# Performance work log

Measured on AMD Instinct MI355X. Metric: run time of the kernel, lower is better.

## Reference

```python
import jax, jax.numpy as jnp
import numpy as np

CHUNK_LEN = 32
N_HEAD = 32
HEAD_SIZE = 64
EPS = 1e-5 * 64.0  # GroupNorm eps = 1e-5 * head_size_divisor**2
PREC_MIN = 0.005   # rwkv_inner precision_min_val clamp for fp32


def rwkv_inner(r, k, v, w, u, kv_state, chunk_len):
    # r,k,v,w: [B,H,L,K]; u: [H,K]; kv_state: [B,H,K,V]
    B, H, L, K = k.shape
    T = chunk_len
    N = L // T
    w = jnp.clip(w, PREC_MIN, None)
    wc_log = jnp.log(w).reshape(B, H, N, T, K)
    wc_cum = jnp.cumsum(wc_log, axis=-2)                      # [B,H,N,T,K]
    shifted = jnp.concatenate([jnp.zeros_like(wc_cum[..., :1, :]), wc_cum[..., :-1, :]], axis=-2)
    ws_log = jnp.sum(wc_log, axis=-2, keepdims=True)          # [B,H,N,1,K]
    w_inter = jnp.exp(ws_log - wc_cum)                        # decay to end of chunk
    w_intra = jnp.exp(wc_cum - wc_log)                        # decay from start of chunk
    rc = r.reshape(B, H, N, T, K)
    kc = k.reshape(B, H, N, T, K)
    vc = v.reshape(B, H, N, T, K)
    # intra-chunk attention, log-space offset at T//2 for numerical stability
    off = shifted[..., T // 2:T // 2 + 1, :]
    r_decay = jnp.exp(shifted - off)
    k_inv_decay = jnp.exp(off - wc_cum)
    a = jnp.einsum('bhntk,bhnsk->bhnts', rc * r_decay, kc * k_inv_decay)
    a = jnp.tril(a, -1)
    diag = jnp.einsum('bhntk,bhntk->bhnt', rc, u[None, :, None, None, :] * kc)
    out = jnp.einsum('bhnts,bhnsv->bhntv', a, vc) + diag[..., None] * vc
    # per-chunk (k*w_inter)^T @ v contributions, then sequential state carry
    wkv = jnp.einsum('bhntk,bhntv->bhnkv', kc * w_inter, vc)  # [B,H,N,K,V]
    ws = jnp.exp(ws_log)[:, :, :, 0, :]                       # [B,H,N,K]

    def step(state, xs):
        ws_i, wkv_i = xs
        new_state = state * ws_i[..., None] + wkv_i
        return new_state, state

    final_state, states = jax.lax.scan(step, kv_state, (jnp.moveaxis(ws, 2, 0), jnp.moveaxis(wkv, 2, 0)))
    states = jnp.moveaxis(states, 0, 2)                       # [B,H,N,K,V]
    out = out + jnp.einsum('bhntk,bhnkv->bhntv', rc * w_intra, states)
    return out.reshape(B, H, L, K), final_state


def _forward(x, shift_state, wkv_state,
             time_maa_x, time_maa_w, time_maa_k, time_maa_v, time_maa_r, time_maa_g,
             time_maa_w1, time_maa_w2, time_decay, time_decay_w1, time_decay_w2,
             time_faaaa, Wr, Wk, Wv, Wg, Wo, gn_w, gn_b):
    B, T, C = x.shape
    H, K = N_HEAD, HEAD_SIZE
    xprev = jnp.concatenate([shift_state[:, None, :], x[:, :-1]], axis=1)
    dx = xprev - x
    # token-shift LoRA mixing
    xxx = jnp.tanh((x + dx * time_maa_x) @ time_maa_w1).reshape(B, T, 5, -1)
    m = jnp.einsum('btfe,fec->fbtc', xxx, time_maa_w2)  # [5,B,T,C]
    mw, mk, mv, mr, mg = m[0], m[1], m[2], m[3], m[4]
    xk = x + dx * (time_maa_k + mk)
    xv = x + dx * (time_maa_v + mv)
    xr = x + dx * (time_maa_r + mr)
    xg = x + dx * (time_maa_g + mg)
    xw = x + dx * (time_maa_w + mw)
    r = (xr @ Wr.T).reshape(B, T, H, K).transpose(0, 2, 1, 3)
    k = (xk @ Wk.T).reshape(B, T, H, K).transpose(0, 2, 1, 3)
    v = (xv @ Wv.T).reshape(B, T, H, K).transpose(0, 2, 1, 3)
    g = jax.nn.silu(xg @ Wg.T)
    w = time_decay.reshape(1, H, 1, K) + (jnp.tanh(xw @ time_decay_w1) @ time_decay_w2).reshape(B, T, H, K).transpose(0, 2, 1, 3)
    w = jnp.exp(-jnp.exp(w))
    out, wkv_out = rwkv_inner(r, k, v, w, time_faaaa, wkv_state, CHUNK_LEN)
    out = out.transpose(0, 2, 1, 3).reshape(B, T, C)
    # GroupNorm with H groups of K channels
    og = out.reshape(B, T, H, K)
    mu = og.mean(-1, keepdims=True)
    var = og.var(-1, keepdims=True)
    og = (og - mu) * jax.lax.rsqrt(var + EPS)
    out = og.reshape(B, T, C) * gn_w + gn_b
    out = (out * g) @ Wo.T
    return out, x[:, -1], wkv_out


def setup_inputs() -> dict:
    B, T, C = 4, 2048, 2048
    H, K = N_HEAD, HEAD_SIZE
    E5, TD = 32, 64
    key = jax.random.key(0)
    ks = jax.random.split(key, 24)
    f32 = jnp.float32
    inp = {
        'x': jax.random.normal(ks[0], (B, T, C), f32),
        'shift_state': jax.random.normal(ks[1], (B, C), f32),
        'wkv_state': jax.random.normal(ks[2], (B, H, K, K), f32) * 0.1,
        'time_maa_x': jax.random.uniform(ks[3], (1, 1, C), f32),
        'time_maa_w': jax.random.uniform(ks[4], (1, 1, C), f32),
        'time_maa_k': jax.random.uniform(ks[5], (1, 1, C), f32),
        'time_maa_v': jax.random.uniform(ks[6], (1, 1, C), f32),
        'time_maa_r': jax.random.uniform(ks[7], (1, 1, C), f32),
        'time_maa_g': jax.random.uniform(ks[8], (1, 1, C), f32),
        'time_maa_w1': jax.random.uniform(ks[9], (C, E5 * 5), f32, -1e-4, 1e-4),
        'time_maa_w2': jax.random.normal(ks[10], (5, E5, C), f32) * 0.01,
        'time_decay': jnp.linspace(-6.0, -1.0, C, dtype=f32).reshape(1, 1, C),
        'time_decay_w1': jax.random.uniform(ks[11], (C, TD), f32, -1e-4, 1e-4),
        'time_decay_w2': jax.random.normal(ks[12], (TD, C), f32) * 0.01,
        'time_faaaa': jax.random.normal(ks[13], (H, K), f32) * 0.1,
        'Wr': jax.random.normal(ks[14], (C, C), f32) * 0.02,
        'Wk': jax.random.normal(ks[15], (C, C), f32) * 0.02,
        'Wv': jax.random.normal(ks[16], (C, C), f32) * 0.02,
        'Wg': jax.random.normal(ks[17], (C, C), f32) * 0.02,
        'Wo': jax.random.normal(ks[18], (C, C), f32) * 0.02,
        'gn_w': jnp.ones((C,), f32),
        'gn_b': jnp.zeros((C,), f32),
    }
    return inp


def reference(x, shift_state, wkv_state,
              time_maa_x, time_maa_w, time_maa_k, time_maa_v, time_maa_r, time_maa_g,
              time_maa_w1, time_maa_w2, time_decay, time_decay_w1, time_decay_w2,
              time_faaaa, Wr, Wk, Wv, Wg, Wo, gn_w, gn_b):
    return _forward(x, shift_state, wkv_state,
                    time_maa_x, time_maa_w, time_maa_k, time_maa_v, time_maa_r, time_maa_g,
                    time_maa_w1, time_maa_w2, time_decay, time_decay_w1, time_decay_w2,
                    time_faaaa, Wr, Wk, Wv, Wg, Wo, gn_w, gn_b)
```

## Files before the change

### kernel.cpp

```cpp
#include <hip/hip_runtime.h>
#include <stdint.h>
#include <math.h>


typedef __attribute__((ext_vector_type(8))) short bf16x8;
typedef __attribute__((ext_vector_type(4))) float f32x4;

#define AS1(p) ((const __attribute__((address_space(1))) void*)(p))
#define AS3(p) ((__attribute__((address_space(3))) void*)(p))

__device__ __forceinline__ unsigned short f2bf(float f) {
  unsigned int u = __builtin_bit_cast(unsigned int, f);
  u += 0x7fffu + ((u >> 16) & 1u);
  return (unsigned short)(u >> 16);
}
__device__ __forceinline__ float bf2f(unsigned short s) {
  unsigned int u = ((unsigned int)s) << 16;
  return __builtin_bit_cast(float, u);
}

template <int EPI, bool BOUNDS>
__global__ __launch_bounds__(256) void gemm_nt(
    const unsigned short* __restrict__ A, const unsigned short* __restrict__ B,
    void* __restrict__ Cp, int M, int N, int K, const float* __restrict__ evec,
    int slot)
{
  __shared__ __align__(16) unsigned short As[128 * 32];
  __shared__ __align__(16) unsigned short Bs[128 * 32];
  const int tid = threadIdx.x;
  const int l = tid & 63, w = tid >> 6;
  const int wm = w & 1, wn = w >> 1;
  const int lm = l & 15, quad = l >> 4;
  const long mBase = (long)blockIdx.y * 128;
  const long nBase = (long)blockIdx.x * 128;

  f32x4 acc[4][4];
  f32x4 zero = {0.f, 0.f, 0.f, 0.f};
#pragma unroll
  for (int i = 0; i < 4; i++)
#pragma unroll
    for (int j = 0; j < 4; j++) acc[i][j] = zero;

  for (int k0 = 0; k0 < K; k0 += 32) {
    if (!BOUNDS) {
      const int r0 = w * 32;
      const int lr = l >> 2, lc = l & 3;
      const unsigned short* gA = A + (mBase + r0 + lr) * (long)K + k0 + lc * 8;
      __builtin_amdgcn_global_load_lds(AS1(gA), AS3(&As[r0 * 32]), 16, 0, 0);
      const unsigned short* gA2 = gA + 16 * (long)K;
      __builtin_amdgcn_global_load_lds(AS1(gA2), AS3(&As[(r0 + 16) * 32]), 16, 0, 0);
      const unsigned short* gB = B + (nBase + r0 + lr) * (long)K + k0 + lc * 8;
      __builtin_amdgcn_global_load_lds(AS1(gB), AS3(&Bs[r0 * 32]), 16, 0, 0);
      const unsigned short* gB2 = gB + 16 * (long)K;
      __builtin_amdgcn_global_load_lds(AS1(gB2), AS3(&Bs[(r0 + 16) * 32]), 16, 0, 0);
    } else {
      const int row = tid >> 2, ch = tid & 3;
#pragma unroll
      for (int rr = 0; rr < 128; rr += 64) {
        int r = rr + row;
        *(int4*)&As[r * 32 + ch * 8] =
            *(const int4*)&A[(mBase + r) * (long)K + k0 + ch * 8];
        int4 bv = make_int4(0, 0, 0, 0);
        long nG = nBase + r;
        if (nG < N) bv = *(const int4*)&B[nG * (long)K + k0 + ch * 8];
        *(int4*)&Bs[r * 32 + ch * 8] = bv;
      }
    }
    __syncthreads();
    bf16x8 af[4], bq[4];
#pragma unroll
    for (int i = 0; i < 4; i++)
      af[i] = *(const bf16x8*)&As[(wm * 64 + i * 16 + lm) * 32 + quad * 8];
#pragma unroll
    for (int i = 0; i < 4; i++)
      bq[i] = *(const bf16x8*)&Bs[(wn * 64 + i * 16 + lm) * 32 + quad * 8];
#pragma unroll
    for (int mi = 0; mi < 4; mi++)
#pragma unroll
      for (int ni = 0; ni < 4; ni++)
        acc[mi][ni] = __builtin_amdgcn_mfma_f32_16x16x32_bf16(af[mi], bq[ni], acc[mi][ni], 0, 0, 0);
    __syncthreads();
  }

#pragma unroll
  for (int mi = 0; mi < 4; mi++) {
#pragma unroll
    for (int ni = 0; ni < 4; ni++) {
      long col = nBase + wn * 64 + ni * 16 + lm;
      if (BOUNDS && col >= N) continue;
      long rw0 = mBase + wm * 64 + mi * 16 + quad * 4;
#pragma unroll
      for (int r = 0; r < 4; r++) {
        float y = acc[mi][ni][r];
        long row = rw0 + r;
        long off = row * (long)N + col;
        if constexpr (EPI == 0) {
          ((float*)Cp)[off] = y;
        } else if constexpr (EPI == 2) {
          ((unsigned short*)Cp)[off] = f2bf(tanhf(y));
        } else if constexpr (EPI == 3) {
          ((unsigned short*)Cp)[off] = f2bf(y / (1.f + __expf(-y)));
        } else if constexpr (EPI == 4) {
          float wv = evec[col] + y;
          ((_Float16*)Cp)[off] = (_Float16)fmaxf(-__expf(wv), -5.2983174f);
        } else if constexpr (EPI == 5) {
          int b = (int)(row >> 11), t = (int)(row & 2047);
          int n = t >> 5, tt = t & 31;
          int h = (int)(col >> 6), kk = (int)(col & 63);
          long c = ((long)(b * 32 + h)) * 64 + n;
          ((unsigned short*)Cp)[c * 6144 + slot + tt * 64 + kk] = f2bf(y);
        }
      }
    }
  }
}

__global__ __launch_bounds__(256) void k_convert(const float* __restrict__ s,
                                                 unsigned short* __restrict__ d, int n4)
{
  int i = blockIdx.x * 256 + threadIdx.x;
  if (i >= n4) return;
  float4 v = ((const float4*)s)[i];
  short4 o;
  o.x = (short)f2bf(v.x); o.y = (short)f2bf(v.y);
  o.z = (short)f2bf(v.z); o.w = (short)f2bf(v.w);
  ((short4*)d)[i] = o;
}

__global__ __launch_bounds__(256) void k_transpose(const float* __restrict__ s,
                                                   unsigned short* __restrict__ d, int R, int C)
{
  int i = blockIdx.x * 256 + threadIdx.x;
  if (i >= R * C) return;
  int r = i / C, c = i - r * C;
  d[(long)c * R + r] = f2bf(s[i]);
}

__global__ __launch_bounds__(256) void k_prep(const float* __restrict__ x,
                                              const float* __restrict__ shift,
                                              const float* __restrict__ maax,
                                              unsigned short* __restrict__ xmix,
                                              float* __restrict__ xlast)
{
  int i = blockIdx.x * 256 + threadIdx.x;
  int c4 = (i & 511) * 4;
  long bt = i >> 9;
  int t = (int)(bt & 2047);
  long b = bt >> 11;
  float4 xv = *(const float4*)&x[bt * 2048 + c4];
  float4 xp;
  if (t == 0) xp = *(const float4*)&shift[b * 2048 + c4];
  else        xp = *(const float4*)&x[(bt - 1) * 2048 + c4];
  float4 mx = *(const float4*)&maax[c4];
  short4 o;
  o.x = (short)f2bf(xv.x + (xp.x - xv.x) * mx.x);
  o.y = (short)f2bf(xv.y + (xp.y - xv.y) * mx.y);
  o.z = (short)f2bf(xv.z + (xp.z - xv.z) * mx.z);
  o.w = (short)f2bf(xv.w + (xp.w - xv.w) * mx.w);
  *(short4*)&xmix[bt * 2048 + c4] = o;
  if (t == 2047) *(float4*)&xlast[b * 2048 + c4] = xv;
}

__global__ __launch_bounds__(256) void k_mix1(
    const unsigned short* __restrict__ xxx, const unsigned short* __restrict__ w2t,
    const float* __restrict__ x, const float* __restrict__ shift,
    const float* __restrict__ maa, unsigned short* __restrict__ xout, int f)
{
  __shared__ __align__(16) unsigned short As[128 * 32];
  __shared__ __align__(16) unsigned short Bs[128 * 32];
  const int tid = threadIdx.x;
  const int l = tid & 63, w = tid >> 6;
  const int wm = w & 1, wn = w >> 1;
  const int lm = l & 15, quad = l >> 4;
  const long mBase = (long)blockIdx.y * 128;
  const long nBase = (long)blockIdx.x * 128;
  const int row = tid >> 2, ch = tid & 3;
#pragma unroll
  for (int rr = 0; rr < 128; rr += 64) {
    int r = rr + row;
    *(int4*)&As[r * 32 + ch * 8] =
        *(const int4*)&xxx[(mBase + r) * 160 + f * 32 + ch * 8];
    *(int4*)&Bs[r * 32 + ch * 8] =
        *(const int4*)&w2t[((long)f * 2048 + nBase + r) * 32 + ch * 8];
  }
  __syncthreads();
  f32x4 zero = {0.f, 0.f, 0.f, 0.f};
  f32x4 acc[4][4];
#pragma unroll
  for (int i = 0; i < 4; i++)
#pragma unroll
    for (int j = 0; j < 4; j++) acc[i][j] = zero;
  bf16x8 af[4], bq[4];
#pragma unroll
  for (int i = 0; i < 4; i++)
    af[i] = *(const bf16x8*)&As[(wm * 64 + i * 16 + lm) * 32 + quad * 8];
#pragma unroll
  for (int i = 0; i < 4; i++)
    bq[i] = *(const bf16x8*)&Bs[(wn * 64 + i * 16 + lm) * 32 + quad * 8];
#pragma unroll
  for (int mi = 0; mi < 4; mi++)
#pragma unroll
    for (int ni = 0; ni < 4; ni++)
      acc[mi][ni] = __builtin_amdgcn_mfma_f32_16x16x32_bf16(af[mi], bq[ni], acc[mi][ni], 0, 0, 0);

#pragma unroll
  for (int mi = 0; mi < 4; mi++) {
#pragma unroll
    for (int ni = 0; ni < 4; ni++) {
      long col = nBase + wn * 64 + ni * 16 + lm;
#pragma unroll
      for (int r = 0; r < 4; r++) {
        long rg = mBase + wm * 64 + mi * 16 + quad * 4 + r;
        int t = (int)(rg & 2047);
        long b = rg >> 11;
        float xval = x[rg * 2048 + col];
        float xp = t ? x[(rg - 1) * 2048 + col] : shift[b * 2048 + col];
        float res = xval + (xp - xval) * (maa[col] + acc[mi][ni][r]);
        xout[rg * 2048 + col] = f2bf(res);
      }
    }
  }
}

__global__ __launch_bounds__(256) void k_chunk(
    unsigned short* __restrict__ recs, const _Float16* __restrict__ wl,
    const float* __restrict__ u, float* __restrict__ outw,
    float* __restrict__ wsb)
{
  const int chunk = blockIdx.x;
  const int n = chunk & 63, bh = chunk >> 6;
  const int h = bh & 31, b = bh >> 5;
  const int tid = threadIdx.x;
  const int lane = tid & 63, wvid = tid >> 6;
  const long rec = (long)chunk * 6144;
  const long tbase = ((long)(b * 2048 + n * 32)) * 2048 + h * 64;

  __shared__ float vc[32][65];
  __shared__ float wcum[32][65];
  __shared__ float rdec[32][65];
  __shared__ float kdec[32][65];
  __shared__ float amat[32][33];
  __shared__ float wsk[64];

  float rcr[8], kcr[8];
#pragma unroll
  for (int j = 0; j < 8; j++) {
    int t = wvid + 4 * j;
    long g = rec + t * 64 + lane;
    rcr[j] = bf2f(recs[g]);
    kcr[j] = bf2f(recs[g + 2048]);
    vc[t][lane] = bf2f(recs[g + 4096]);
    wcum[t][lane] = (float)wl[tbase + (long)t * 2048 + lane];
  }
  float uval = u[h * 64 + lane];
  __syncthreads();

  if (tid < 64) {
    float run = 0.f;
    for (int t = 0; t < 32; t++) { run += wcum[t][tid]; wcum[t][tid] = run; }
    wsk[tid] = run;
  }
  __syncthreads();

  const float offv = wcum[15][lane];
  const float wsv = wsk[lane];
  float rdr[8], kdr[8], klr[8], rwir[8], dpart[8];
#pragma unroll
  for (int j = 0; j < 8; j++) {
    int t = wvid + 4 * j;
    float cw = wcum[t][lane];
    float sh = t ? wcum[t - 1][lane] : 0.f;
    rwir[j] = rcr[j] * __expf(sh);
    rdr[j] = rcr[j] * __expf(sh - offv);
    kdr[j] = kcr[j] * __expf(offv - cw);
    klr[j] = kcr[j] * __expf(wsv - cw);
    dpart[j] = rcr[j] * uval * kcr[j];
  }
  __syncthreads();

#pragma unroll
  for (int j = 0; j < 8; j++) {
    int t = wvid + 4 * j;
    rdec[t][lane] = rdr[j];
    kdec[t][lane] = kdr[j];
    wcum[t][lane] = klr[j];
    recs[rec + 4096 + t * 64 + lane] = f2bf(rwir[j]);
  }
  if (tid < 64) wsb[(long)chunk * 64 + tid] = __expf(wsk[tid]);
  __syncthreads();

  {
    const int t0 = (tid >> 4) * 2, s0 = (tid & 15) * 2;
    float a00 = 0, a01 = 0, a10 = 0, a11 = 0;
    for (int kk = 0; kk < 64; kk++) {
      float r0 = rdec[t0][kk], r1 = rdec[t0 + 1][kk];
      float c0 = kdec[s0][kk], c1 = kdec[s0 + 1][kk];
      a00 += r0 * c0; a01 += r0 * c1; a10 += r1 * c0; a11 += r1 * c1;
    }
    amat[t0][s0]         = (s0     < t0)     ? a00 : 0.f;
    amat[t0][s0 + 1]     = (s0 + 1 < t0)     ? a01 : 0.f;
    amat[t0 + 1][s0]     = (s0     < t0 + 1) ? a10 : 0.f;
    amat[t0 + 1][s0 + 1] = (s0 + 1 < t0 + 1) ? a11 : 0.f;
  }
  __syncthreads();
#pragma unroll
  for (int j = 0; j < 8; j++) {
    float d = dpart[j];
#pragma unroll
    for (int m = 32; m; m >>= 1) d += __shfl_xor(d, m, 64);
    if (lane == 0) amat[wvid + 4 * j][wvid + 4 * j] = d;
  }
  __syncthreads();

  {
    const int t0 = (tid >> 4) * 2, v0 = (tid & 15) * 4;
    float o00 = 0, o01 = 0, o02 = 0, o03 = 0, o10 = 0, o11 = 0, o12 = 0, o13 = 0;
    for (int s = 0; s < 32; s++) {
      float a0 = amat[t0][s], a1 = amat[t0 + 1][s];
      float b0 = vc[s][v0], b1 = vc[s][v0 + 1], b2 = vc[s][v0 + 2], b3 = vc[s][v0 + 3];
      o00 += a0 * b0; o01 += a0 * b1; o02 += a0 * b2; o03 += a0 * b3;
      o10 += a1 * b0; o11 += a1 * b1; o12 += a1 * b2; o13 += a1 * b3;
    }
    float* p0 = &outw[tbase + (long)t0 * 2048 + v0];
    float* p1 = &outw[tbase + (long)(t0 + 1) * 2048 + v0];
    p0[0] = o00; p0[1] = o01; p0[2] = o02; p0[3] = o03;
    p1[0] = o10; p1[1] = o11; p1[2] = o12; p1[3] = o13;
  }

  {
    const int kk0 = (tid >> 4) * 4, v0 = (tid & 15) * 4;
    float a[4][4];
#pragma unroll
    for (int i = 0; i < 4; i++)
#pragma unroll
      for (int j = 0; j < 4; j++) a[i][j] = 0.f;
    for (int t = 0; t < 32; t++) {
      float w0 = wcum[t][kk0], w1 = wcum[t][kk0 + 1], w2 = wcum[t][kk0 + 2], w3 = wcum[t][kk0 + 3];
      float b0 = vc[t][v0], b1 = vc[t][v0 + 1], b2 = vc[t][v0 + 2], b3 = vc[t][v0 + 3];
      a[0][0] += w0 * b0; a[0][1] += w0 * b1; a[0][2] += w0 * b2; a[0][3] += w0 * b3;
      a[1][0] += w1 * b0; a[1][1] += w1 * b1; a[1][2] += w1 * b2; a[1][3] += w1 * b3;
      a[2][0] += w2 * b0; a[2][1] += w2 * b1; a[2][2] += w2 * b2; a[2][3] += w2 * b3;
      a[3][0] += w3 * b0; a[3][1] += w3 * b1; a[3][2] += w3 * b2; a[3][3] += w3 * b3;
    }
#pragma unroll
    for (int i = 0; i < 4; i++)
#pragma unroll
      for (int j = 0; j < 4; j++)
        recs[rec + (kk0 + i) * 64 + v0 + j] = f2bf(a[i][j]);
  }
}

__global__ __launch_bounds__(256) void k_scan(unsigned short* __restrict__ recs,
                                              const float* __restrict__ wsb,
                                              const float* __restrict__ kv0,
                                              float* __restrict__ finalst)
{
  const int bh = blockIdx.x >> 2;
  const int kq = blockIdx.x & 3;
  const int tid = threadIdx.x;
  float st[4];
  const long base = (long)bh * 4096 + kq * 1024;
#pragma unroll
  for (int j = 0; j < 4; j++) st[j] = kv0[base + j * 256 + tid];
  for (int n = 0; n < 64; n++) {
    const long cb = ((long)bh * 64 + n) * 6144 + kq * 1024;
    const long wb = ((long)bh * 64 + n) * 64 + kq * 16;
#pragma unroll
    for (int j = 0; j < 4; j++) {
      int i = j * 256 + tid;
      unsigned short* p = &recs[cb + i];
      float wv = bf2f(*p);
      *p = f2bf(st[j]);
      st[j] = st[j] * wsb[wb + (i >> 6)] + wv;
    }
  }
#pragma unroll
  for (int j = 0; j < 4; j++) finalst[base + j * 256 + tid] = st[j];
}

__global__ __launch_bounds__(256) void k_inter(const unsigned short* __restrict__ recs,
                                               float* __restrict__ outw)
{
  const int chunk = blockIdx.x;
  const int n = chunk & 63, bh = chunk >> 6;
  const int h = bh & 31, b = bh >> 5;
  const int tid = threadIdx.x;
  __shared__ float st[64][65];
  __shared__ float rw[32][65];
  const long rec = (long)chunk * 6144;
  for (int i = tid; i < 4096; i += 256) st[i >> 6][i & 63] = bf2f(recs[rec + i]);
  for (int i = tid; i < 2048; i += 256) rw[i >> 6][i & 63] = bf2f(recs[rec + 4096 + i]);
  __syncthreads();
  const long tbase = ((long)(b * 2048 + n * 32)) * 2048 + h * 64;
  const int t0 = (tid >> 4) * 2, v0 = (tid & 15) * 4;
  float o00 = 0, o01 = 0, o02 = 0, o03 = 0, o10 = 0, o11 = 0, o12 = 0, o13 = 0;
  for (int kk = 0; kk < 64; kk++) {
    float r0 = rw[t0][kk], r1 = rw[t0 + 1][kk];
    float s0 = st[kk][v0], s1 = st[kk][v0 + 1], s2 = st[kk][v0 + 2], s3 = st[kk][v0 + 3];
    o00 += r0 * s0; o01 += r0 * s1; o02 += r0 * s2; o03 += r0 * s3;
    o10 += r1 * s0; o11 += r1 * s1; o12 += r1 * s2; o13 += r1 * s3;
  }
  float* p0 = &outw[tbase + (long)t0 * 2048 + v0];
  float* p1 = &outw[tbase + (long)(t0 + 1) * 2048 + v0];
  p0[0] += o00; p0[1] += o01; p0[2] += o02; p0[3] += o03;
  p1[0] += o10; p1[1] += o11; p1[2] += o12; p1[3] += o13;
}

__global__ __launch_bounds__(256) void k_gnorm(const float* __restrict__ outw,
                                               const unsigned short* __restrict__ gb,
                                               const float* __restrict__ gnw,
                                               const float* __restrict__ gnb,
                                               unsigned short* __restrict__ aout)
{
  const int gid = blockIdx.x * 4 + (threadIdx.x >> 6);
  const int lane = threadIdx.x & 63;
  const long bt = gid >> 5;
  const int h = gid & 31;
  const int c = h * 64 + lane;
  const long off = bt * 2048 + c;
  float y = outw[off];
  float s = y, sq = y * y;
#pragma unroll
  for (int m = 32; m; m >>= 1) {
    s += __shfl_xor(s, m, 64);
    sq += __shfl_xor(sq, m, 64);
  }
  float mu = s * (1.f / 64.f);
  float var = sq * (1.f / 64.f) - mu * mu;
  float nrm = (y - mu) * rsqrtf(var + 6.4e-4f);
  float o = (nrm * gnw[c] + gnb[c]) * bf2f(gb[off]);
  aout[off] = f2bf(o);
}

extern "C" void kernel_launch(void* const* d_in, const int* in_sizes, int n_in,
                              void* d_out, int out_size, void* d_ws, size_t ws_size,
                              hipStream_t stream)
{
  const float* x     = (const float*)d_in[0];
  const float* shift = (const float*)d_in[1];
  const float* kv0   = (const float*)d_in[2];
  const float* maax  = (const float*)d_in[3];
  const float* maaw  = (const float*)d_in[4];
  const float* maak  = (const float*)d_in[5];
  const float* maav  = (const float*)d_in[6];
  const float* maar  = (const float*)d_in[7];
  const float* maag  = (const float*)d_in[8];
  const float* w1    = (const float*)d_in[9];
  const float* w2    = (const float*)d_in[10];
  const float* tdec  = (const float*)d_in[11];
  const float* tdw1  = (const float*)d_in[12];
  const float* tdw2  = (const float*)d_in[13];
  const float* u     = (const float*)d_in[14];
  const float* Wr    = (const float*)d_in[15];
  const float* Wk    = (const float*)d_in[16];
  const float* Wv    = (const float*)d_in[17];
  const float* Wg    = (const float*)d_in[18];
  const float* Wo    = (const float*)d_in[19];
  const float* gnw   = (const float*)d_in[20];
  const float* gnb   = (const float*)d_in[21];

  char* ws = (char*)d_ws;
  const size_t MB = 1048576;
  unsigned short* WbfR  = (unsigned short*)(ws + 0 * MB);
  unsigned short* WbfK  = (unsigned short*)(ws + 8 * MB);
  unsigned short* WbfV  = (unsigned short*)(ws + 16 * MB);
  unsigned short* WbfG  = (unsigned short*)(ws + 24 * MB);
  unsigned short* WbfO  = (unsigned short*)(ws + 32 * MB);
  unsigned short* w2tb  = (unsigned short*)(ws + 40 * MB);
  unsigned short* w1t   = (unsigned short*)(ws + 40 * MB + 655360);
  unsigned short* tdw1t = (unsigned short*)(ws + 40 * MB + 1310720);
  unsigned short* tdw2t = (unsigned short*)(ws + 40 * MB + 1572864);
  unsigned short* xxxb  = (unsigned short*)(ws + 40 * MB + 1835008);
  unsigned short* t1b   = (unsigned short*)(ws + 40 * MB + 4456448);
  float*          wsb   = (float*)(ws + 40 * MB + 5505024);
  unsigned short* xmixb = (unsigned short*)(ws + 48 * MB);
  _Float16*       wlb   = (_Float16*)(ws + 48 * MB);
  unsigned short* x1b   = (unsigned short*)(ws + 80 * MB);
  unsigned short* aob   = (unsigned short*)(ws + 80 * MB);
  unsigned short* recs  = (unsigned short*)(ws + 112 * MB);
  unsigned short* gbuf  = recs;

  float* outp    = (float*)d_out;
  float* xlast   = outp + 16777216;
  float* finalst = outp + 16777216 + 8192;

  k_convert<<<4096, 256, 0, stream>>>(Wr, WbfR, 1048576);
  k_convert<<<4096, 256, 0, stream>>>(Wk, WbfK, 1048576);
  k_convert<<<4096, 256, 0, stream>>>(Wv, WbfV, 1048576);
  k_convert<<<4096, 256, 0, stream>>>(Wg, WbfG, 1048576);
  k_convert<<<4096, 256, 0, stream>>>(Wo, WbfO, 1048576);
  k_transpose<<<1280, 256, 0, stream>>>(w1, w1t, 2048, 160);
  k_transpose<<<512, 256, 0, stream>>>(tdw1, tdw1t, 2048, 64);
  k_transpose<<<512, 256, 0, stream>>>(tdw2, tdw2t, 64, 2048);
  for (int f = 0; f < 5; f++)
    k_transpose<<<256, 256, 0, stream>>>(w2 + (long)f * 65536, w2tb + (long)f * 65536, 32, 2048);

  k_prep<<<16384, 256, 0, stream>>>(x, shift, maax, xmixb, xlast);
  gemm_nt<2, true><<<dim3(2, 64), 256, 0, stream>>>(xmixb, w1t, xxxb, 8192, 160, 2048, nullptr, 0);

  k_mix1<<<dim3(16, 64), 256, 0, stream>>>(xxxb, w2tb, x, shift, maaw, x1b, 0);
  gemm_nt<2, true><<<dim3(1, 64), 256, 0, stream>>>(x1b, tdw1t, t1b, 8192, 64, 2048, nullptr, 0);
  gemm_nt<4, false><<<dim3(16, 64), 256, 0, stream>>>(t1b, tdw2t, wlb, 8192, 2048, 64, tdec, 0);
  k_mix1<<<dim3(16, 64), 256, 0, stream>>>(xxxb, w2tb, x, shift, maak, x1b, 1);
  gemm_nt<5, false><<<dim3(16, 64), 256, 0, stream>>>(x1b, WbfK, recs, 8192, 2048, 2048, nullptr, 2048);
  k_mix1<<<dim3(16, 64), 256, 0, stream>>>(xxxb, w2tb, x, shift, maav, x1b, 2);
  gemm_nt<5, false><<<dim3(16, 64), 256, 0, stream>>>(x1b, WbfV, recs, 8192, 2048, 2048, nullptr, 4096);
  k_mix1<<<dim3(16, 64), 256, 0, stream>>>(xxxb, w2tb, x, shift, maar, x1b, 3);
  gemm_nt<5, false><<<dim3(16, 64), 256, 0, stream>>>(x1b, WbfR, recs, 8192, 2048, 2048, nullptr, 0);
  k_mix1<<<dim3(16, 64), 256, 0, stream>>>(xxxb, w2tb, x, shift, maag, x1b, 4);

  k_chunk<<<8192, 256, 0, stream>>>(recs, wlb, u, outp, wsb);
  k_scan<<<512, 256, 0, stream>>>(recs, wsb, kv0, finalst);
  k_inter<<<8192, 256, 0, stream>>>(recs, outp);

  gemm_nt<3, false><<<dim3(16, 64), 256, 0, stream>>>(x1b, WbfG, gbuf, 8192, 2048, 2048, nullptr, 0);
  k_gnorm<<<65536, 256, 0, stream>>>(outp, gbuf, gnw, gnb, aob);
  gemm_nt<0, false><<<dim3(16, 64), 256, 0, stream>>>(aob, WbfO, outp, 8192, 2048, 2048, nullptr, 0);
}
```

Measured before the change: 1.361 ms.

## Add 256x256-tile double-buffered GEMM kernel for the five large projections

Adds a new 512-thread GEMM kernel with 256x256 output tiles, a K-step of 64, and double-buffered LDS filled through direct global-to-LDS loads using a swizzled layout. It interleaves MFMA work with prefetch of the next stage and raises wave priority around the MFMA blocks. The R/K/V/G/O projection GEMMs now use it in place of the 128-tile kernel. The aim is more data reuse per tile and better overlap of loads with compute. The cost is high register and LDS use, which allows only one block per CU, and a grid of 256 blocks that may underfill the device.

```diff
diff --git a/kernel.cpp b/kernel.cpp
--- a/kernel.cpp
+++ b/kernel.cpp
@@ -108,6 +108,131 @@
           int n = t >> 5, tt = t & 31;
           int h = (int)(col >> 6), kk = (int)(col & 63);
           long c = ((long)(b * 32 + h)) * 64 + n;
+          ((unsigned short*)Cp)[c * 6144 + slot + tt * 64 + kk] = f2bf(y);
+        }
+      }
+    }
+  }
+}
+
+template <int EPI>
+__global__ __launch_bounds__(512, 1) void gemm256_nt(
+    const unsigned short* __restrict__ A, const unsigned short* __restrict__ B,
+    void* __restrict__ Cp, int M, int N, int K, int slot)
+{
+  __shared__ __align__(16) unsigned short As2[2][16384];
+  __shared__ __align__(16) unsigned short Bs2[2][16384];
+  const int tid = threadIdx.x;
+  const int l = tid & 63;
+  const int w = tid >> 6;
+  const int wm = w >> 2, wn = w & 3;
+  const int lm = l & 15, quad = l >> 4;
+  const long mBase = (long)blockIdx.y * 256;
+  const long nBase = (long)blockIdx.x * 256;
+  const int NT = K >> 6;
+
+  const int r0 = tid >> 3;
+  const int csw = (tid & 7) ^ (r0 & 7);
+  const int ldsOff = (tid & ~63) * 8;
+  const unsigned short* ga0 = A + (mBase + r0) * (long)K + csw * 8;
+  const unsigned short* gb0 = B + (nBase + r0) * (long)K + csw * 8;
+
+  f32x4 acc[8][4];
+  f32x4 zero = {0.f, 0.f, 0.f, 0.f};
+#pragma unroll
+  for (int i = 0; i < 8; i++)
+#pragma unroll
+    for (int j = 0; j < 4; j++) acc[i][j] = zero;
+
+#define STAGE256(kt_)                                                          \
+  {                                                                            \
+    const int _b = (kt_) & 1;                                                  \
+    const unsigned short* _ga = ga0 + (long)(kt_) * 64;                        \
+    const unsigned short* _gb = gb0 + (long)(kt_) * 64;                        \
+    __builtin_amdgcn_global_load_lds(AS1(_ga), AS3(&As2[_b][ldsOff]), 16, 0, 0);              \
+    __builtin_amdgcn_global_load_lds(AS1(_gb), AS3(&Bs2[_b][ldsOff]), 16, 0, 0);              \
+    __builtin_amdgcn_global_load_lds(AS1(_ga + (long)64 * K), AS3(&As2[_b][4096 + ldsOff]), 16, 0, 0);  \
+    __builtin_amdgcn_global_load_lds(AS1(_gb + (long)64 * K), AS3(&Bs2[_b][4096 + ldsOff]), 16, 0, 0);  \
+    __builtin_amdgcn_global_load_lds(AS1(_ga + (long)128 * K), AS3(&As2[_b][8192 + ldsOff]), 16, 0, 0); \
+    __builtin_amdgcn_global_load_lds(AS1(_gb + (long)128 * K), AS3(&Bs2[_b][8192 + ldsOff]), 16, 0, 0); \
+    __builtin_amdgcn_global_load_lds(AS1(_ga + (long)192 * K), AS3(&As2[_b][12288 + ldsOff]), 16, 0, 0);\
+    __builtin_amdgcn_global_load_lds(AS1(_gb + (long)192 * K), AS3(&Bs2[_b][12288 + ldsOff]), 16, 0, 0);\
+  }
+
+  STAGE256(0);
+  STAGE256(1);
+  asm volatile("s_waitcnt vmcnt(8)" ::: "memory");
+  __builtin_amdgcn_s_barrier();
+
+  const int q0 = (quad ^ (lm & 7)) * 8;
+  const int rA = (wm * 128 + lm) * 64;
+  const int rB = (wn * 64 + lm) * 64;
+
+  for (int kt = 0; kt < NT; ++kt) {
+    const int b = kt & 1;
+    bf16x8 af[8][2], bq[4][2];
+#pragma unroll
+    for (int fm = 0; fm < 8; fm++)
+      af[fm][0] = *(const bf16x8*)&As2[b][rA + fm * 1024 + q0];
+#pragma unroll
+    for (int fn = 0; fn < 4; fn++)
+      bq[fn][0] = *(const bf16x8*)&Bs2[b][rB + fn * 1024 + q0];
+#pragma unroll
+    for (int fm = 0; fm < 8; fm++)
+      af[fm][1] = *(const bf16x8*)&As2[b][rA + fm * 1024 + (q0 ^ 32)];
+#pragma unroll
+    for (int fn = 0; fn < 4; fn++)
+      bq[fn][1] = *(const bf16x8*)&Bs2[b][rB + fn * 1024 + (q0 ^ 32)];
+
+    __builtin_amdgcn_s_setprio(1);
+#pragma unroll
+    for (int fm = 0; fm < 8; fm++)
+#pragma unroll
+      for (int fn = 0; fn < 4; fn++)
+        acc[fm][fn] = __builtin_amdgcn_mfma_f32_16x16x32_bf16(af[fm][0], bq[fn][0], acc[fm][fn], 0, 0, 0);
+    __builtin_amdgcn_s_setprio(0);
+
+    asm volatile("s_waitcnt lgkmcnt(0)" ::: "memory");
+    __builtin_amdgcn_s_barrier();
+    if (kt + 2 < NT) STAGE256(kt + 2);
+
+    __builtin_amdgcn_s_setprio(1);
+#pragma unroll
+    for (int fm = 0; fm < 8; fm++)
+#pragma unroll
+      for (int fn = 0; fn < 4; fn++)
+        acc[fm][fn] = __builtin_amdgcn_mfma_f32_16x16x32_bf16(af[fm][1], bq[fn][1], acc[fm][fn], 0, 0, 0);
+    __builtin_amdgcn_s_setprio(0);
+
+    if (kt + 2 < NT) {
+      asm volatile("s_waitcnt vmcnt(8)" ::: "memory");
+    } else {
+      asm volatile("s_waitcnt vmcnt(0)" ::: "memory");
+    }
+    __builtin_amdgcn_s_barrier();
+  }
+#undef STAGE256
+
+#pragma unroll
+  for (int mi = 0; mi < 8; mi++) {
+#pragma unroll
+    for (int ni = 0; ni < 4; ni++) {
+      long col = nBase + wn * 64 + ni * 16 + lm;
+      long rw0 = mBase + wm * 128 + mi * 16 + quad * 4;
+#pragma unroll
+      for (int r = 0; r < 4; r++) {
+        float y = acc[mi][ni][r];
+        long row = rw0 + r;
+        long off = row * (long)N + col;
+        if constexpr (EPI == 0) {
+          ((float*)Cp)[off] = y;
+        } else if constexpr (EPI == 3) {
+          ((unsigned short*)Cp)[off] = f2bf(y / (1.f + __expf(-y)));
+        } else if constexpr (EPI == 5) {
+          int bb = (int)(row >> 11), t = (int)(row & 2047);
+          int n = t >> 5, tt = t & 31;
+          int h = (int)(col >> 6), kk = (int)(col & 63);
+          long c = ((long)(bb * 32 + h)) * 64 + n;
           ((unsigned short*)Cp)[c * 6144 + slot + tt * 64 + kk] = f2bf(y);
         }
       }
@@ -502,18 +627,18 @@
   gemm_nt<2, true><<<dim3(1, 64), 256, 0, stream>>>(x1b, tdw1t, t1b, 8192, 64, 2048, nullptr, 0);
   gemm_nt<4, false><<<dim3(16, 64), 256, 0, stream>>>(t1b, tdw2t, wlb, 8192, 2048, 64, tdec, 0);
   k_mix1<<<dim3(16, 64), 256, 0, stream>>>(xxxb, w2tb, x, shift, maak, x1b, 1);
-  gemm_nt<5, false><<<dim3(16, 64), 256, 0, stream>>>(x1b, WbfK, recs, 8192, 2048, 2048, nullptr, 2048);
+  gemm256_nt<5><<<dim3(8, 32), 512, 0, stream>>>(x1b, WbfK, recs, 8192, 2048, 2048, 2048);
   k_mix1<<<dim3(16, 64), 256, 0, stream>>>(xxxb, w2tb, x, shift, maav, x1b, 2);
-  gemm_nt<5, false><<<dim3(16, 64), 256, 0, stream>>>(x1b, WbfV, recs, 8192, 2048, 2048, nullptr, 4096);
+  gemm256_nt<5><<<dim3(8, 32), 512, 0, stream>>>(x1b, WbfV, recs, 8192, 2048, 2048, 4096);
   k_mix1<<<dim3(16, 64), 256, 0, stream>>>(xxxb, w2tb, x, shift, maar, x1b, 3);
-  gemm_nt<5, false><<<dim3(16, 64), 256, 0, stream>>>(x1b, WbfR, recs, 8192, 2048, 2048, nullptr, 0);
+  gemm256_nt<5><<<dim3(8, 32), 512, 0, stream>>>(x1b, WbfR, recs, 8192, 2048, 2048, 0);
   k_mix1<<<dim3(16, 64), 256, 0, stream>>>(xxxb, w2tb, x, shift, maag, x1b, 4);
 
   k_chunk<<<8192, 256, 0, stream>>>(recs, wlb, u, outp, wsb);
   k_scan<<<512, 256, 0, stream>>>(recs, wsb, kv0, finalst);
   k_inter<<<8192, 256, 0, stream>>>(recs, outp);
 
-  gemm_nt<3, false><<<dim3(16, 64), 256, 0, stream>>>(x1b, WbfG, gbuf, 8192, 2048, 2048, nullptr, 0);
+  gemm256_nt<3><<<dim3(8, 32), 512, 0, stream>>>(x1b, WbfG, gbuf, 8192, 2048, 2048, 0);
   k_gnorm<<<65536, 256, 0, stream>>>(outp, gbuf, gnw, gnb, aob);
-  gemm_nt<0, false><<<dim3(16, 64), 256, 0, stream>>>(aob, WbfO, outp, 8192, 2048, 2048, nullptr, 0);
-}
+  gemm256_nt<0><<<dim3(8, 32), 512, 0, stream>>>(aob, WbfO, outp, 8192, 2048, 2048, 0);
+}
```

After: 1.281 ms. -5.8%, faster.
